# Kernel tuning notes

Hardware: AMD Instinct MI355X
Metric: run time of the kernel (lower is better)

## Reference

```python
import jax, jax.numpy as jnp
import numpy as np

N = 8192       # node_number
D = 64         # embed_dim
S = 4096       # number of triad samples
BETA0 = 0.1
BETA1 = 0.1
MARGIN = 1.0
EPS = 1e-6
P_EDGE = 0.004  # edge density -> avg degree ~33


def setup_inputs() -> dict:
    key = jax.random.key(0)
    k1, k2, k3, k4, k5, k6, k7, k8, k9, k10 = jax.random.split(key, 10)
    emb_t = jax.random.normal(k1, (N, D), dtype=jnp.float32) * 0.05
    emb_prev = jax.random.normal(k2, (N, D), dtype=jnp.float32) * 0.05
    theta = jax.random.normal(k3, (N, D), dtype=jnp.float32) * 0.05
    edge_mask = jax.random.uniform(k4, (N, N)) < P_EDGE
    adj = jnp.where(edge_mask, jax.random.uniform(k5, (N, N), dtype=jnp.float32), 0.0)
    j_idx = jax.random.randint(k6, (S,), 0, N, dtype=jnp.int32)
    k_idx = jax.random.randint(k7, (S,), 0, N, dtype=jnp.int32)
    negj_idx = jax.random.randint(k8, (S,), 0, N, dtype=jnp.int32)
    i_idx = jax.random.randint(k9, (S,), 0, N, dtype=jnp.int32)
    condition = jax.random.randint(k10, (S,), -1, 2, dtype=jnp.int32)  # {-1,0,1}
    return {
        "emb_t": emb_t, "emb_prev": emb_prev, "theta": theta, "adj": adj,
        "j_idx": j_idx, "k_idx": k_idx, "negj_idx": negj_idx,
        "i_idx": i_idx, "condition": condition,
    }


def _loss(emb_t, emb_prev, theta, adj, j_idx, k_idx, negj_idx, i_idx, condition):
    E = emb_t
    # ---- L_sh: triplet hinge, per sample ----
    uj, uk, unj = E[j_idx], E[k_idx], E[negj_idx]          # [S, D]
    pos = jnp.sum((uj - uk) ** 2, axis=-1)                  # [S]
    neg = jnp.sum((unj - uk) ** 2, axis=-1)                 # [S]
    L_sh = jnp.sum(jax.nn.relu(pos - neg + MARGIN))
    # ---- L_tr: common-neighbor closure loss ----
    # dot(s, l) = theta_l . x(i,j,l) where x = adj[i,l]*(u_l-u_i) + adj[j,l]*(u_l-u_j)
    Ai = adj[i_idx]                                         # [S, N] gather of adj rows
    Aj = adj[j_idx]                                         # [S, N]
    diag = jnp.sum(theta * E, axis=-1)                      # [N]  theta_l . u_l
    ui = E[i_idx]                                           # [S, D]
    ti = ui @ theta.T                                       # [S, N]  theta_l . u_i
    tj = uj @ theta.T                                       # [S, N]  theta_l . u_j
    dots = Ai * (diag[None, :] - ti) + Aj * (diag[None, :] - tj)  # [S, N]
    # P = sigmoid(dot), with the original power>100 cutoff (power = -dot)
    P_all = jnp.where(dots < -100.0, 0.0, jax.nn.sigmoid(dots))
    cn_mask = (Ai > 0) & (Aj > 0)                           # common neighbors of (i, j)
    C1 = 1.0 - jnp.prod(jnp.where(cn_mask, 1.0 - P_all, 1.0), axis=1)  # [S]
    dot_k = jnp.take_along_axis(dots, k_idx[:, None].astype(jnp.int32), axis=1)[:, 0]  # [S]
    C0 = jnp.where(dot_k < -100.0, 0.0, jax.nn.sigmoid(dot_k))
    C = 1.0 - C0 / (C1 + EPS)
    log_p = jax.nn.softplus(-dot_k)                         # log(1 + exp(-theta_k.x))
    vest = jnp.where(condition == 1, C, dot_k)
    ltr = jnp.where(condition == -1, 0.0, log_p + vest)
    L_tr = jnp.sum(ltr)
    # ---- L_smooth: added once per sample (timestamp strictly between 0 and graph_number) ----
    n_samples = jnp.float32(j_idx.shape[0])
    L_smooth = n_samples * jnp.sum((emb_t - emb_prev) ** 2)
    return L_sh + BETA0 * L_tr + BETA1 * L_smooth


def reference(emb_t, emb_prev, theta, adj, j_idx, k_idx, negj_idx, i_idx, condition):
    return _loss(emb_t, emb_prev, theta, adj, j_idx, k_idx, negj_idx, i_idx, condition)
```

## Files before the change

kernel.cpp:

```cpp
#include <hip/hip_runtime.h>
#include <math.h>

#define NN 8192
#define DD 64
#define SS 4096

__device__ __forceinline__ float wred(float v) {
    #pragma unroll
    for (int o = 1; o < 64; o <<= 1) v += __shfl_xor(v, o);
    return v;
}

__global__ void __launch_bounds__(64) fused_sample_kernel(
        const float* __restrict__ E, const float* __restrict__ Eprev,
        const float* __restrict__ theta, const float* __restrict__ adj,
        const int* __restrict__ j_idx, const int* __restrict__ k_idx,
        const int* __restrict__ nj_idx, const int* __restrict__ i_idx,
        const int* __restrict__ cond, float4* __restrict__ part) {
    int s = blockIdx.x;
    int lane = threadIdx.x;

    int j = j_idx[s], k = k_idx[s], nj = nj_idx[s], i = i_idx[s], c = cond[s];

    float ui  = E[(size_t)i  * DD + lane];
    float uj  = E[(size_t)j  * DD + lane];
    float uk  = E[(size_t)k  * DD + lane];
    float un  = E[(size_t)nj * DD + lane];
    float thk = theta[(size_t)k * DD + lane];

    float dp = uj - uk, dn = un - uk;
    float pos = wred(dp * dp);
    float neg = wred(dn * dn);
    float tik = wred(thk * ui);
    float tjk = wred(thk * uj);
    float dgk = wred(thk * uk);

    float sm;
    {
        const float2* a2 = (const float2*)E;
        const float2* b2 = (const float2*)Eprev;
        float2 x = a2[(size_t)s * 64 + lane];
        float2 y = b2[(size_t)s * 64 + lane];
        float dx = x.x - y.x, dy = x.y - y.y;
        sm = wred(dx * dx + dy * dy);
    }

    float prod = 1.0f;
    if (c == 1) {
        const float4* ri = (const float4*)(adj + (size_t)i * NN);
        const float4* rj = (const float4*)(adj + (size_t)j * NN);
        for (int it = 0; it < 8; ++it) {
            float4 A[4], B[4];
            #pragma unroll
            for (int u = 0; u < 4; ++u) {
                A[u] = ri[(it * 4 + u) * 64 + lane];
                B[u] = rj[(it * 4 + u) * 64 + lane];
            }
            #pragma unroll
            for (int u = 0; u < 4; ++u) {
                float av[4] = {A[u].x, A[u].y, A[u].z, A[u].w};
                float bv[4] = {B[u].x, B[u].y, B[u].z, B[u].w};
                #pragma unroll
                for (int q = 0; q < 4; ++q) {
                    unsigned long long m = __ballot(av[q] > 0.f && bv[q] > 0.f);
                    while (m) {
                        int src = __ffsll((unsigned long long)m) - 1;
                        m &= m - 1;
                        float ai = __shfl(av[q], src);
                        float aj = __shfl(bv[q], src);
                        int l = ((it * 4 + u) * 64 + src) * 4 + q;
                        float th = theta[(size_t)l * DD + lane];
                        float ul = E[(size_t)l * DD + lane];
                        float r1 = wred(th * (ul - ui));
                        float r2 = wred(th * (ul - uj));
                        float dl = ai * r1 + aj * r2;
                        float P = (dl < -100.f) ? 0.f : 1.f / (1.f + __expf(-dl));
                        prod *= (1.f - P);
                    }
                }
            }
        }
    }

    if (lane == 0) {
        float lsh = fmaxf(pos - neg + 1.0f, 0.f);

        float aik = adj[(size_t)i * NN + k];
        float ajk = adj[(size_t)j * NN + k];
        float dot_k = aik * (dgk - tik) + ajk * (dgk - tjk);

        float x = -dot_k;
        float logp = fmaxf(x, 0.f) + log1pf(expf(-fabsf(x)));

        float ltr;
        if (c == -1) {
            ltr = 0.f;
        } else if (c == 0) {
            ltr = logp + dot_k;
        } else {
            float C1 = 1.f - prod;
            float C0 = (dot_k < -100.f) ? 0.f : 1.f / (1.f + expf(-dot_k));
            ltr = logp + (1.f - C0 / (C1 + 1e-6f));
        }
        part[s] = make_float4(lsh, ltr, sm, 0.f);
    }
}

__global__ void __launch_bounds__(256) final_reduce_kernel(
        const float4* __restrict__ part, float* __restrict__ out) {
    double lsh = 0.0, ltr = 0.0, sm = 0.0;
    for (int t = threadIdx.x; t < SS; t += 256) {
        float4 p = part[t];
        lsh += (double)p.x;
        ltr += (double)p.y;
        sm  += (double)p.z;
    }
    #pragma unroll
    for (int o = 32; o; o >>= 1) {
        lsh += __shfl_down(lsh, o);
        ltr += __shfl_down(ltr, o);
        sm  += __shfl_down(sm, o);
    }
    __shared__ double sh[3][4];
    int lane = threadIdx.x & 63, wv = threadIdx.x >> 6;
    if (lane == 0) { sh[0][wv] = lsh; sh[1][wv] = ltr; sh[2][wv] = sm; }
    __syncthreads();
    if (threadIdx.x == 0) {
        double L = (sh[0][0] + sh[0][1] + sh[0][2] + sh[0][3])
                 + 0.1 * (sh[1][0] + sh[1][1] + sh[1][2] + sh[1][3])
                 + 0.1 * (double)SS * (sh[2][0] + sh[2][1] + sh[2][2] + sh[2][3]);
        out[0] = (float)L;
    }
}

extern "C" void kernel_launch(void* const* d_in, const int* in_sizes, int n_in,
                              void* d_out, int out_size, void* d_ws, size_t ws_size,
                              hipStream_t stream) {
    const float* emb_t    = (const float*)d_in[0];
    const float* emb_prev = (const float*)d_in[1];
    const float* theta    = (const float*)d_in[2];
    const float* adj      = (const float*)d_in[3];
    const int*   j_idx    = (const int*)d_in[4];
    const int*   k_idx    = (const int*)d_in[5];
    const int*   nj_idx   = (const int*)d_in[6];
    const int*   i_idx    = (const int*)d_in[7];
    const int*   cond     = (const int*)d_in[8];
    float* out = (float*)d_out;

    float4* part = (float4*)d_ws;

    fused_sample_kernel<<<SS, 64, 0, stream>>>(
        emb_t, emb_prev, theta, adj, j_idx, k_idx, nj_idx, i_idx, cond, part);
    final_reduce_kernel<<<1, 256, 0, stream>>>(part, out);
}
```

Before: 343.1 us.

## Sort heavy samples first and read only the i-row when finding common neighbors

A partition kernel reorders samples with an atomic counter so the heavy condition==1 samples are scheduled first, to reduce tail imbalance. The common-neighbor search now streams only adj row i, compacts its nonzeros into shared memory, and then gathers only those columns of row j. This roughly halves the dense row bandwidth for each heavy sample. It adds a memset and an extra kernel launch, and it truncates at 512 neighbors per row, which holds for average degree ~33.

```diff
diff --git a/kernel.cpp b/kernel.cpp
--- a/kernel.cpp
+++ b/kernel.cpp
@@ -4,6 +4,7 @@
 #define NN 8192
 #define DD 64
 #define SS 4096
+#define CAP 512
 
 __device__ __forceinline__ float wred(float v) {
     #pragma unroll
@@ -11,13 +12,28 @@
     return v;
 }
 
+
+__global__ void __launch_bounds__(256) partition_kernel(
+        const int* __restrict__ cond, int* __restrict__ counters,
+        int* __restrict__ order) {
+    int t = blockIdx.x * 256 + threadIdx.x;
+    if (t < SS) {
+        int c = cond[t];
+        int p;
+        if (c == 1) p = atomicAdd(&counters[0], 1);
+        else        p = SS - 1 - atomicAdd(&counters[1], 1);
+        order[p] = t;
+    }
+}
+
 __global__ void __launch_bounds__(64) fused_sample_kernel(
         const float* __restrict__ E, const float* __restrict__ Eprev,
         const float* __restrict__ theta, const float* __restrict__ adj,
         const int* __restrict__ j_idx, const int* __restrict__ k_idx,
         const int* __restrict__ nj_idx, const int* __restrict__ i_idx,
-        const int* __restrict__ cond, float4* __restrict__ part) {
-    int s = blockIdx.x;
+        const int* __restrict__ cond, const int* __restrict__ order,
+        float4* __restrict__ part) {
+    int s = order[blockIdx.x];
     int lane = threadIdx.x;
 
     int j = j_idx[s], k = k_idx[s], nj = nj_idx[s], i = i_idx[s], c = cond[s];
@@ -27,6 +43,9 @@
     float uk  = E[(size_t)k  * DD + lane];
     float un  = E[(size_t)nj * DD + lane];
     float thk = theta[(size_t)k * DD + lane];
+
+    float aik = adj[(size_t)i * NN + k];
+    float ajk = adj[(size_t)j * NN + k];
 
     float dp = uj - uk, dn = un - uk;
     float pos = wred(dp * dp);
@@ -47,37 +66,56 @@
 
     float prod = 1.0f;
     if (c == 1) {
+        __shared__ int   idx_sh[CAP];
+        __shared__ float aval_sh[CAP];
+        __shared__ float bval_sh[CAP];
+
         const float4* ri = (const float4*)(adj + (size_t)i * NN);
-        const float4* rj = (const float4*)(adj + (size_t)j * NN);
-        for (int it = 0; it < 8; ++it) {
-            float4 A[4], B[4];
+        int cnt = 0;
+
+        for (int it = 0; it < 4; ++it) {
+            float4 A[8];
             #pragma unroll
-            for (int u = 0; u < 4; ++u) {
-                A[u] = ri[(it * 4 + u) * 64 + lane];
-                B[u] = rj[(it * 4 + u) * 64 + lane];
-            }
+            for (int u = 0; u < 8; ++u)
+                A[u] = ri[(it * 8 + u) * 64 + lane];
             #pragma unroll
-            for (int u = 0; u < 4; ++u) {
+            for (int u = 0; u < 8; ++u) {
                 float av[4] = {A[u].x, A[u].y, A[u].z, A[u].w};
-                float bv[4] = {B[u].x, B[u].y, B[u].z, B[u].w};
                 #pragma unroll
                 for (int q = 0; q < 4; ++q) {
-                    unsigned long long m = __ballot(av[q] > 0.f && bv[q] > 0.f);
-                    while (m) {
-                        int src = __ffsll((unsigned long long)m) - 1;
-                        m &= m - 1;
-                        float ai = __shfl(av[q], src);
-                        float aj = __shfl(bv[q], src);
-                        int l = ((it * 4 + u) * 64 + src) * 4 + q;
-                        float th = theta[(size_t)l * DD + lane];
-                        float ul = E[(size_t)l * DD + lane];
-                        float r1 = wred(th * (ul - ui));
-                        float r2 = wred(th * (ul - uj));
-                        float dl = ai * r1 + aj * r2;
-                        float P = (dl < -100.f) ? 0.f : 1.f / (1.f + __expf(-dl));
-                        prod *= (1.f - P);
+                    bool hit = av[q] > 0.f;
+                    unsigned long long m = __ballot(hit);
+                    if (hit) {
+                        int off = __popcll(m & ((1ull << lane) - 1ull));
+                        int p = cnt + off;
+                        if (p < CAP) {
+                            idx_sh[p]  = ((it * 8 + u) * 64 + lane) * 4 + q;
+                            aval_sh[p] = av[q];
+                        }
                     }
+                    cnt += __popcll(m);
                 }
+            }
+        }
+        if (cnt > CAP) cnt = CAP;
+        __syncthreads();
+
+        for (int p = lane; p < cnt; p += 64)
+            bval_sh[p] = adj[(size_t)j * NN + idx_sh[p]];
+        __syncthreads();
+
+        for (int p = 0; p < cnt; ++p) {
+            float bj = bval_sh[p];
+            if (bj > 0.f) {
+                int l = idx_sh[p];
+                float ai = aval_sh[p];
+                float th = theta[(size_t)l * DD + lane];
+                float ul = E[(size_t)l * DD + lane];
+                float r1 = wred(th * (ul - ui));
+                float r2 = wred(th * (ul - uj));
+                float dl = ai * r1 + bj * r2;
+                float P = (dl < -100.f) ? 0.f : 1.f / (1.f + __expf(-dl));
+                prod *= (1.f - P);
             }
         }
     }
@@ -85,8 +123,6 @@
     if (lane == 0) {
         float lsh = fmaxf(pos - neg + 1.0f, 0.f);
 
-        float aik = adj[(size_t)i * NN + k];
-        float ajk = adj[(size_t)j * NN + k];
         float dot_k = aik * (dgk - tik) + ajk * (dgk - tjk);
 
         float x = -dot_k;
@@ -147,9 +183,14 @@
     const int*   cond     = (const int*)d_in[8];
     float* out = (float*)d_out;
 
-    float4* part = (float4*)d_ws;
+    int*    counters = (int*)d_ws;
+    int*    order    = (int*)((char*)d_ws + 16);
+    float4* part     = (float4*)((char*)d_ws + 16 + 4 * SS);
 
+    hipMemsetAsync(d_ws, 0, 16, stream);
+    partition_kernel<<<SS / 256, 256, 0, stream>>>(cond, counters, order);
     fused_sample_kernel<<<SS, 64, 0, stream>>>(
-        emb_t, emb_prev, theta, adj, j_idx, k_idx, nj_idx, i_idx, cond, part);
+        emb_t, emb_prev, theta, adj, j_idx, k_idx, nj_idx, i_idx, cond,
+        order, part);
     final_reduce_kernel<<<1, 256, 0, stream>>>(part, out);
 }
```

After: 340.6 us. No clear change (-0.7%).
